# Kernel tuning notes

Hardware: AMD Instinct MI355X
Metric: run time of the kernel (lower is better)

Reference implementation:

```python
import jax, jax.numpy as jnp
import numpy as np

N_NODES = 50000
N_EDGES = 600000
N_FEAT = 128
N_GRAPHS = 256
DIM = 95
N_OUT = 12
N_ITER = 10
BN_EPS = 1e-5


def setup_inputs() -> dict:
    key = jax.random.key(0)
    ks = jax.random.split(key, 16)
    inp = {}
    inp["x"] = jax.random.normal(ks[0], (N_NODES, N_FEAT), dtype=jnp.float32)
    inp["edge_index"] = jax.random.randint(ks[1], (2, N_EDGES), 0, N_NODES, dtype=jnp.int64)
    inp["batch"] = jnp.sort(jax.random.randint(ks[2], (N_NODES,), 0, N_GRAPHS, dtype=jnp.int64))
    def lin(k, fan_in, fan_out):
        bound = 1.0 / np.sqrt(fan_in)
        kw, kb = jax.random.split(k)
        W = jax.random.uniform(kw, (fan_in, fan_out), jnp.float32, -bound, bound)
        b = jax.random.uniform(kb, (fan_out,), jnp.float32, -bound, bound)
        return W, b
    inp["W1a"], inp["b1a"] = lin(ks[3], N_FEAT, N_FEAT)            # nn1 layer 1
    inp["W1b"], inp["b1b"] = lin(ks[4], N_FEAT, N_FEAT)            # nn1 layer 2
    inp["gamma"] = jnp.ones((N_FEAT,), jnp.float32)                 # bn1 weight
    inp["beta"] = jnp.zeros((N_FEAT,), jnp.float32)                 # bn1 bias
    inp["Wl1"], inp["bl1"] = lin(ks[5], 2 * N_FEAT, N_FEAT // 2)   # lin1
    inp["Wl2"], inp["bl2"] = lin(ks[6], 2 * N_FEAT, N_FEAT // 2)   # lin2
    inp["Wm1"], inp["bm1"] = lin(ks[7], N_FEAT, DIM)               # MLP layer 1
    inp["Wm2"], inp["bm2"] = lin(ks[8], DIM, N_OUT)                # MLP layer 2
    return inp


def reference(x, edge_index, batch, W1a, b1a, W1b, b1b, gamma, beta,
              Wl1, bl1, Wl2, bl2, Wm1, bm1, Wm2, bm2):
    src, dst = edge_index[0], edge_index[1]
    # GINConv (eps=0): h_i = nn1(x_i + sum_{j->i} x_j)
    agg = jax.ops.segment_sum(x[src], dst, num_segments=N_NODES)
    h0 = x + agg
    h0 = jax.nn.relu(h0 @ W1a + b1a) @ W1b + b1b
    x1 = jax.nn.relu(h0)
    # BatchNorm1d (training mode: batch statistics, biased variance)
    mean = jnp.mean(x1, axis=0)
    var = jnp.mean(jnp.square(x1 - mean), axis=0)
    x1 = gamma * (x1 - mean) * jax.lax.rsqrt(var + BN_EPS) + beta
    # global_mean_pool over graph ids
    sums = jax.ops.segment_sum(x1, batch, num_segments=N_GRAPHS)
    counts = jax.ops.segment_sum(jnp.ones((N_NODES,), x1.dtype), batch, num_segments=N_GRAPHS)
    xg = sums / jnp.maximum(counts, 1.0)[:, None]
    # recurrent gated loop
    h = xg
    for _ in range(N_ITER):
        cat = jnp.concatenate([xg, h], axis=1)          # [G, 2*F]
        p = cat @ Wl1 + bl1
        q = cat @ Wl2 + bl2
        h = jnp.concatenate([jnp.tanh(q), jax.nn.sigmoid(p)], axis=1)
    # output MLP
    return jax.nn.relu(h @ Wm1 + bm1) @ Wm2 + bm2
```

## Files before the change

kernel.cpp:

```cpp
#include <hip/hip_runtime.h>
#include <cstddef>

#define N_NODES  50000
#define N_EDGES  600000
#define N_FEAT   128
#define N_GRAPHS 256
#define DIMM     95
#define N_OUTD   12
#define N_ITERS  10

#define N_CHUNKS 196

#define WS_BUF   0
#define WS_STATS (N_NODES * N_FEAT)
#define WS_SCALE (WS_STATS + 256)
#define WS_XG    (WS_SCALE + 256)
#define WS_CNT   (WS_XG + N_GRAPHS * N_FEAT)
#define WS_OFF   (WS_CNT + N_NODES)
#define WS_CUR   (WS_OFF + N_NODES + 4)
#define WS_CHS   (WS_CUR + N_NODES)
#define WS_SORT  (WS_CHS + 256)

#define SR 132

__global__ void k_zero(float* __restrict__ ws) {
    int i = blockIdx.x * 256 + threadIdx.x;
    int* cnt = (int*)ws + WS_CNT;
    if (i < N_NODES) cnt[i] = 0;
    if (blockIdx.x == 0) ws[WS_STATS + threadIdx.x] = 0.f;
}

__global__ void k_hist(const int* __restrict__ ei, float* __restrict__ ws) {
    int e = blockIdx.x * 256 + threadIdx.x;
    int* cnt = (int*)ws + WS_CNT;
    if (e < N_EDGES) atomicAdd(&cnt[ei[N_EDGES + e]], 1);
}

__global__ void k_chunk(float* __restrict__ ws) {
    __shared__ int red[4];
    const int tid = threadIdx.x;
    int* cnt = (int*)ws + WS_CNT;
    int i = blockIdx.x * 256 + tid;
    int v = (i < N_NODES) ? cnt[i] : 0;
    #pragma unroll
    for (int d = 32; d; d >>= 1) v += __shfl_down(v, d);
    if ((tid & 63) == 0) red[tid >> 6] = v;
    __syncthreads();
    if (tid == 0) ((int*)ws + WS_CHS)[blockIdx.x] = red[0] + red[1] + red[2] + red[3];
}

__global__ void k_scan0(float* __restrict__ ws) {
    __shared__ int s[256];
    const int tid = threadIdx.x;
    int* chs = (int*)ws + WS_CHS;
    int v = (tid < N_CHUNKS) ? chs[tid] : 0;
    s[tid] = v;
    __syncthreads();
    #pragma unroll
    for (int d = 1; d < 256; d <<= 1) {
        int t = (tid >= d) ? s[tid - d] : 0;
        __syncthreads();
        s[tid] += t;
        __syncthreads();
    }
    if (tid < N_CHUNKS) chs[tid] = s[tid] - v;
    if (tid == 0) ((int*)ws + WS_OFF)[N_NODES] = N_EDGES;
}

__global__ void k_scan1(float* __restrict__ ws) {
    __shared__ int s[256];
    const int tid = threadIdx.x;
    int* cnt = (int*)ws + WS_CNT;
    int* off = (int*)ws + WS_OFF;
    int* cur = (int*)ws + WS_CUR;
    int i = blockIdx.x * 256 + tid;
    int v = (i < N_NODES) ? cnt[i] : 0;
    s[tid] = v;
    __syncthreads();
    #pragma unroll
    for (int d = 1; d < 256; d <<= 1) {
        int t = (tid >= d) ? s[tid - d] : 0;
        __syncthreads();
        s[tid] += t;
        __syncthreads();
    }
    int o = ((int*)ws + WS_CHS)[blockIdx.x] + s[tid] - v;
    if (i < N_NODES) { off[i] = o; cur[i] = o; }
}

__global__ void k_scatter(const int* __restrict__ ei, float* __restrict__ ws) {
    int e = blockIdx.x * 256 + threadIdx.x;
    if (e >= N_EDGES) return;
    int d = ei[N_EDGES + e];
    int s = ei[e];
    int* cur = (int*)ws + WS_CUR;
    int pos = atomicAdd(&cur[d], 1);
    ((int*)ws + WS_SORT)[pos] = s;
}

__global__ __launch_bounds__(256, 4) void k_fused(const float* __restrict__ x,
        float* __restrict__ ws,
        const float* __restrict__ W1a, const float* __restrict__ b1a,
        const float* __restrict__ W1b, const float* __restrict__ b1b) {
    __shared__ float As[64 * SR];
    const int tid  = threadIdx.x;
    const int lane = tid & 63;
    const int wv   = tid >> 6;
    const int fg   = tid & 15;
    const int rg   = tid >> 4;
    const int row0 = blockIdx.x * 64;

    const int* off = (const int*)ws + WS_OFF;
    const int* ss  = (const int*)ws + WS_SORT;

    for (int ii = 0; ii < 16; ++ii) {
        const int i = wv * 16 + ii;
        const int r = row0 + i;
        float a0 = 0.f, a1 = 0.f;
        if (r < N_NODES) {
            a0 = x[(size_t)r * N_FEAT + lane];
            a1 = x[(size_t)r * N_FEAT + 64 + lane];
            const int lo = off[r], hi = off[r + 1];
            int e = lo;
            for (; e + 4 <= hi; e += 4) {
                int s0 = ss[e], s1 = ss[e + 1], s2 = ss[e + 2], s3 = ss[e + 3];
                const float* p0 = x + (size_t)s0 * N_FEAT;
                const float* p1 = x + (size_t)s1 * N_FEAT;
                const float* p2 = x + (size_t)s2 * N_FEAT;
                const float* p3 = x + (size_t)s3 * N_FEAT;
                float u0 = p0[lane], v0 = p0[64 + lane];
                float u1 = p1[lane], v1 = p1[64 + lane];
                float u2 = p2[lane], v2 = p2[64 + lane];
                float u3 = p3[lane], v3 = p3[64 + lane];
                a0 += u0 + u1 + u2 + u3;
                a1 += v0 + v1 + v2 + v3;
            }
            for (; e < hi; ++e) {
                const float* p = x + (size_t)ss[e] * N_FEAT;
                a0 += p[lane];
                a1 += p[64 + lane];
            }
        }
        As[i * SR + lane]      = a0;
        As[i * SR + 64 + lane] = a1;
    }
    __syncthreads();

    float acc[4][8];
    #pragma unroll
    for (int i = 0; i < 4; ++i)
        #pragma unroll
        for (int j = 0; j < 8; ++j) acc[i][j] = 0.f;

    #pragma unroll 2
    for (int k = 0; k < N_FEAT; k += 4) {
        float4 w[8];
        #pragma unroll
        for (int kk = 0; kk < 4; ++kk) {
            w[2 * kk]     = *(const float4*)(W1a + (k + kk) * N_FEAT + fg * 8);
            w[2 * kk + 1] = *(const float4*)(W1a + (k + kk) * N_FEAT + fg * 8 + 4);
        }
        #pragma unroll
        for (int i = 0; i < 4; ++i) {
            const float4 a4 = *(const float4*)(As + (rg * 4 + i) * SR + k);
            const float av[4] = {a4.x, a4.y, a4.z, a4.w};
            #pragma unroll
            for (int kk = 0; kk < 4; ++kk) {
                acc[i][0] += av[kk] * w[2 * kk].x;
                acc[i][1] += av[kk] * w[2 * kk].y;
                acc[i][2] += av[kk] * w[2 * kk].z;
                acc[i][3] += av[kk] * w[2 * kk].w;
                acc[i][4] += av[kk] * w[2 * kk + 1].x;
                acc[i][5] += av[kk] * w[2 * kk + 1].y;
                acc[i][6] += av[kk] * w[2 * kk + 1].z;
                acc[i][7] += av[kk] * w[2 * kk + 1].w;
            }
        }
    }
    __syncthreads();

    {
        const float4 ba0 = *(const float4*)(b1a + fg * 8);
        const float4 ba1 = *(const float4*)(b1a + fg * 8 + 4);
        #pragma unroll
        for (int i = 0; i < 4; ++i) {
            float4 u0, u1;
            u0.x = fmaxf(acc[i][0] + ba0.x, 0.f); u0.y = fmaxf(acc[i][1] + ba0.y, 0.f);
            u0.z = fmaxf(acc[i][2] + ba0.z, 0.f); u0.w = fmaxf(acc[i][3] + ba0.w, 0.f);
            u1.x = fmaxf(acc[i][4] + ba1.x, 0.f); u1.y = fmaxf(acc[i][5] + ba1.y, 0.f);
            u1.z = fmaxf(acc[i][6] + ba1.z, 0.f); u1.w = fmaxf(acc[i][7] + ba1.w, 0.f);
            *(float4*)(As + (rg * 4 + i) * SR + fg * 8)     = u0;
            *(float4*)(As + (rg * 4 + i) * SR + fg * 8 + 4) = u1;
        }
    }
    __syncthreads();

    #pragma unroll
    for (int i = 0; i < 4; ++i)
        #pragma unroll
        for (int j = 0; j < 8; ++j) acc[i][j] = 0.f;

    #pragma unroll 2
    for (int k = 0; k < N_FEAT; k += 4) {
        float4 w[8];
        #pragma unroll
        for (int kk = 0; kk < 4; ++kk) {
            w[2 * kk]     = *(const float4*)(W1b + (k + kk) * N_FEAT + fg * 8);
            w[2 * kk + 1] = *(const float4*)(W1b + (k + kk) * N_FEAT + fg * 8 + 4);
        }
        #pragma unroll
        for (int i = 0; i < 4; ++i) {
            const float4 a4 = *(const float4*)(As + (rg * 4 + i) * SR + k);
            const float av[4] = {a4.x, a4.y, a4.z, a4.w};
            #pragma unroll
            for (int kk = 0; kk < 4; ++kk) {
                acc[i][0] += av[kk] * w[2 * kk].x;
                acc[i][1] += av[kk] * w[2 * kk].y;
                acc[i][2] += av[kk] * w[2 * kk].z;
                acc[i][3] += av[kk] * w[2 * kk].w;
                acc[i][4] += av[kk] * w[2 * kk + 1].x;
                acc[i][5] += av[kk] * w[2 * kk + 1].y;
                acc[i][6] += av[kk] * w[2 * kk + 1].z;
                acc[i][7] += av[kk] * w[2 * kk + 1].w;
            }
        }
    }
    {
        float* __restrict__ buf = ws + WS_BUF;
        const float4 bb0 = *(const float4*)(b1b + fg * 8);
        const float4 bb1 = *(const float4*)(b1b + fg * 8 + 4);
        #pragma unroll
        for (int i = 0; i < 4; ++i) {
            int r = row0 + rg * 4 + i;
            if (r < N_NODES) {
                float4 u0, u1;
                u0.x = fmaxf(acc[i][0] + bb0.x, 0.f); u0.y = fmaxf(acc[i][1] + bb0.y, 0.f);
                u0.z = fmaxf(acc[i][2] + bb0.z, 0.f); u0.w = fmaxf(acc[i][3] + bb0.w, 0.f);
                u1.x = fmaxf(acc[i][4] + bb1.x, 0.f); u1.y = fmaxf(acc[i][5] + bb1.y, 0.f);
                u1.z = fmaxf(acc[i][6] + bb1.z, 0.f); u1.w = fmaxf(acc[i][7] + bb1.w, 0.f);
                *(float4*)(buf + (size_t)r * N_FEAT + fg * 8)     = u0;
                *(float4*)(buf + (size_t)r * N_FEAT + fg * 8 + 4) = u1;
            }
        }
    }
}

__global__ void k_stats(const float* __restrict__ buf, float* __restrict__ stats) {
    __shared__ float S[8][128];
    __shared__ float Q[8][128];
    const int tid = threadIdx.x;
    const int cg = tid & 31;
    const int rg = tid >> 5;
    float4 s = make_float4(0.f, 0.f, 0.f, 0.f);
    float4 q = make_float4(0.f, 0.f, 0.f, 0.f);
    for (int r = blockIdx.x * 8 + rg; r < N_NODES; r += gridDim.x * 8) {
        float4 v = *(const float4*)(buf + (size_t)r * N_FEAT + cg * 4);
        s.x += v.x; s.y += v.y; s.z += v.z; s.w += v.w;
        q.x += v.x * v.x; q.y += v.y * v.y; q.z += v.z * v.z; q.w += v.w * v.w;
    }
    S[rg][cg * 4 + 0] = s.x; S[rg][cg * 4 + 1] = s.y;
    S[rg][cg * 4 + 2] = s.z; S[rg][cg * 4 + 3] = s.w;
    Q[rg][cg * 4 + 0] = q.x; Q[rg][cg * 4 + 1] = q.y;
    Q[rg][cg * 4 + 2] = q.z; Q[rg][cg * 4 + 3] = q.w;
    __syncthreads();
    if (tid < 128) {
        float t = 0.f;
        #pragma unroll
        for (int g = 0; g < 8; ++g) t += S[g][tid];
        unsafeAtomicAdd(stats + tid, t);
    } else {
        int c = tid - 128;
        float t = 0.f;
        #pragma unroll
        for (int g = 0; g < 8; ++g) t += Q[g][c];
        unsafeAtomicAdd(stats + 128 + c, t);
    }
}

__global__ void k_finalize(const float* __restrict__ gamma, const float* __restrict__ beta,
                           float* __restrict__ ws) {
    int c = threadIdx.x;
    float mean = ws[WS_STATS + c] * (1.f / N_NODES);
    float var  = fmaxf(ws[WS_STATS + 128 + c] * (1.f / N_NODES) - mean * mean, 0.f);
    float sc = gamma[c] * rsqrtf(var + 1e-5f);
    ws[WS_SCALE + c] = sc;
    ws[WS_SCALE + 128 + c] = beta[c] - mean * sc;
}

__device__ __forceinline__ int lbound(const int* __restrict__ a, int n, int v) {
    int lo = 0, hi = n;
    while (lo < hi) { int m = (lo + hi) >> 1; if (a[m] < v) lo = m + 1; else hi = m; }
    return lo;
}

__global__ void k_pool(const float* __restrict__ buf, const int* __restrict__ batch,
                       float* __restrict__ ws) {
    __shared__ float S[8][128];
    __shared__ int range[2];
    const int g = blockIdx.x, tid = threadIdx.x;
    if (tid == 0) {
        range[0] = lbound(batch, N_NODES, g);
        range[1] = lbound(batch, N_NODES, g + 1);
    }
    __syncthreads();
    const int lo = range[0], hi = range[1];
    const int cg = tid & 31, rg = tid >> 5;
    float4 s = make_float4(0.f, 0.f, 0.f, 0.f);
    for (int r = lo + rg; r < hi; r += 8) {
        float4 v = *(const float4*)(buf + (size_t)r * N_FEAT + cg * 4);
        s.x += v.x; s.y += v.y; s.z += v.z; s.w += v.w;
    }
    S[rg][cg * 4 + 0] = s.x; S[rg][cg * 4 + 1] = s.y;
    S[rg][cg * 4 + 2] = s.z; S[rg][cg * 4 + 3] = s.w;
    __syncthreads();
    if (tid < 128) {
        float t = 0.f;
        #pragma unroll
        for (int g8 = 0; g8 < 8; ++g8) t += S[g8][tid];
        int cnt = hi - lo;
        float sc = ws[WS_SCALE + tid], sh = ws[WS_SCALE + 128 + tid];
        ws[WS_XG + g * N_FEAT + tid] = (cnt > 0) ? (sc * t / (float)cnt + sh) : 0.f;
    }
}

__global__ __launch_bounds__(256) void k_recur(const float* __restrict__ ws,
        const float* __restrict__ Wl1, const float* __restrict__ bl1,
        const float* __restrict__ Wl2, const float* __restrict__ bl2,
        const float* __restrict__ Wm1, const float* __restrict__ bm1,
        const float* __restrict__ Wm2, const float* __restrict__ bm2,
        float* __restrict__ out) {
    __shared__ float W1h[128 * 64];
    __shared__ float W2h[128 * 64];
    __shared__ float xg_s[128];
    __shared__ float h_s[128];
    __shared__ float px[2][64];
    __shared__ float pq[2][2][64];
    __shared__ float m_s[DIMM];
    const int g = blockIdx.x, tid = threadIdx.x;

    for (int i = tid; i < 128 * 64; i += 256) {
        W1h[i] = Wl1[128 * 64 + i];
        W2h[i] = Wl2[128 * 64 + i];
    }
    if (tid < 128) {
        float v = ws[WS_XG + g * N_FEAT + tid];
        xg_s[tid] = v;
        h_s[tid] = v;
    }
    __syncthreads();

    const int sel  = tid >> 7;
    const int part = (tid >> 6) & 1;
    const int j    = tid & 63;

    {
        const float* Wg = sel ? Wl2 : Wl1;
        float a = 0.f;
        const int k0 = part * 64;
        #pragma unroll 4
        for (int k = 0; k < 64; ++k) a += xg_s[k0 + k] * Wg[(k0 + k) * 64 + j];
        pq[sel][part][j] = a;
    }
    __syncthreads();
    if (part == 0) {
        const float* bias = sel ? bl2 : bl1;
        px[sel][j] = pq[sel][0][j] + pq[sel][1][j] + bias[j];
    }
    __syncthreads();

    const float* Wh = sel ? W2h : W1h;
    for (int it = 0; it < N_ITERS; ++it) {
        float a = 0.f;
        const int k0 = part * 64;
        #pragma unroll
        for (int k = 0; k < 64; k += 4) {
            const float4 h4 = *(const float4*)(h_s + k0 + k);
            a += h4.x * Wh[(k0 + k + 0) * 64 + j];
            a += h4.y * Wh[(k0 + k + 1) * 64 + j];
            a += h4.z * Wh[(k0 + k + 2) * 64 + j];
            a += h4.w * Wh[(k0 + k + 3) * 64 + j];
        }
        pq[sel][part][j] = a;
        __syncthreads();
        if (part == 0) {
            float tot = pq[sel][0][j] + pq[sel][1][j] + px[sel][j];
            if (sel == 0) h_s[64 + j] = 1.f / (1.f + expf(-tot));
            else          h_s[j] = tanhf(tot);
        }
        __syncthreads();
    }

    if (tid < DIMM) {
        float a = bm1[tid];
        #pragma unroll 4
        for (int k = 0; k < 128; ++k) a += h_s[k] * Wm1[k * DIMM + tid];
        m_s[tid] = fmaxf(a, 0.f);
    }
    __syncthreads();
    if (tid < N_OUTD) {
        float a = bm2[tid];
        for (int k = 0; k < DIMM; ++k) a += m_s[k] * Wm2[k * N_OUTD + tid];
        out[g * N_OUTD + tid] = a;
    }
}

extern "C" void kernel_launch(void* const* d_in, const int* in_sizes, int n_in,
                              void* d_out, int out_size, void* d_ws, size_t ws_size,
                              hipStream_t stream) {
    const float* x     = (const float*)d_in[0];
    const int*   ei    = (const int*)d_in[1];
    const int*   batch = (const int*)d_in[2];
    const float* W1a = (const float*)d_in[3];
    const float* b1a = (const float*)d_in[4];
    const float* W1b = (const float*)d_in[5];
    const float* b1b = (const float*)d_in[6];
    const float* gamma = (const float*)d_in[7];
    const float* beta  = (const float*)d_in[8];
    const float* Wl1 = (const float*)d_in[9];
    const float* bl1 = (const float*)d_in[10];
    const float* Wl2 = (const float*)d_in[11];
    const float* bl2 = (const float*)d_in[12];
    const float* Wm1 = (const float*)d_in[13];
    const float* bm1 = (const float*)d_in[14];
    const float* Wm2 = (const float*)d_in[15];
    const float* bm2 = (const float*)d_in[16];
    float* out = (float*)d_out;
    float* ws  = (float*)d_ws;

    k_zero   <<<(N_NODES + 255) / 256, 256, 0, stream>>>(ws);
    k_hist   <<<(N_EDGES + 255) / 256, 256, 0, stream>>>(ei, ws);
    k_chunk  <<<N_CHUNKS, 256, 0, stream>>>(ws);
    k_scan0  <<<1, 256, 0, stream>>>(ws);
    k_scan1  <<<N_CHUNKS, 256, 0, stream>>>(ws);
    k_scatter<<<(N_EDGES + 255) / 256, 256, 0, stream>>>(ei, ws);
    k_fused  <<<(N_NODES + 63) / 64, 256, 0, stream>>>(x, ws, W1a, b1a, W1b, b1b);
    k_stats  <<<512, 256, 0, stream>>>(ws + WS_BUF, ws + WS_STATS);
    k_finalize<<<1, 128, 0, stream>>>(gamma, beta, ws);
    k_pool   <<<N_GRAPHS, 256, 0, stream>>>(ws + WS_BUF, batch, ws);
    k_recur  <<<N_GRAPHS, 256, 0, stream>>>(ws, Wl1, bl1, Wl2, bl2, Wm1, bm1, Wm2, bm2, out);
}
```

Baseline: 342.2 us.

## Fuse BN statistics and mean pooling into GIN MLP kernel epilogue

The fused gather+MLP kernel no longer writes the 50000x128 activation buffer. Its epilogue stages the tile in shared memory, accumulates per-feature sum and sum-of-squares, and pools per-graph sums with atomics. BN scale/shift is then applied to the pooled sums in a small kernel, which replaces the separate stats, finalize and pool passes. The gather loop also loads neighbor indices cooperatively per wave with shuffles and float2 loads. This adds atomics and an extra sync, and applying BN after pooling relies on its linearity.

```diff
diff --git a/kernel.cpp b/kernel.cpp
--- a/kernel.cpp
+++ b/kernel.cpp
@@ -11,10 +11,8 @@
 
 #define N_CHUNKS 196
 
-#define WS_BUF   0
-#define WS_STATS (N_NODES * N_FEAT)
-#define WS_SCALE (WS_STATS + 256)
-#define WS_XG    (WS_SCALE + 256)
+#define WS_STATS 0
+#define WS_XG    (WS_STATS + 256)
 #define WS_CNT   (WS_XG + N_GRAPHS * N_FEAT)
 #define WS_OFF   (WS_CNT + N_NODES)
 #define WS_CUR   (WS_OFF + N_NODES + 4)
@@ -27,7 +25,8 @@
     int i = blockIdx.x * 256 + threadIdx.x;
     int* cnt = (int*)ws + WS_CNT;
     if (i < N_NODES) cnt[i] = 0;
-    if (blockIdx.x == 0) ws[WS_STATS + threadIdx.x] = 0.f;
+    if (i < 256) ws[WS_STATS + i] = 0.f;
+    if (i < N_GRAPHS * N_FEAT) ws[WS_XG + i] = 0.f;
 }
 
 __global__ void k_hist(const int* __restrict__ ei, float* __restrict__ ws) {
@@ -99,10 +98,12 @@
 }
 
 __global__ __launch_bounds__(256, 4) void k_fused(const float* __restrict__ x,
-        float* __restrict__ ws,
+        const int* __restrict__ batch, float* __restrict__ ws,
         const float* __restrict__ W1a, const float* __restrict__ b1a,
         const float* __restrict__ W1b, const float* __restrict__ b1b) {
     __shared__ float As[64 * SR];
+    __shared__ float red[256];
+    __shared__ int batch_l[64];
     const int tid  = threadIdx.x;
     const int lane = tid & 63;
     const int wv   = tid >> 6;
@@ -113,36 +114,42 @@
     const int* off = (const int*)ws + WS_OFF;
     const int* ss  = (const int*)ws + WS_SORT;
 
+    if (tid < 64) {
+        int r = row0 + tid;
+        batch_l[tid] = (r < N_NODES) ? batch[r] : (N_GRAPHS - 1);
+    }
+
     for (int ii = 0; ii < 16; ++ii) {
         const int i = wv * 16 + ii;
         const int r = row0 + i;
-        float a0 = 0.f, a1 = 0.f;
+        float2 acc = make_float2(0.f, 0.f);
         if (r < N_NODES) {
-            a0 = x[(size_t)r * N_FEAT + lane];
-            a1 = x[(size_t)r * N_FEAT + 64 + lane];
+            acc = *(const float2*)(x + (size_t)r * N_FEAT + 2 * lane);
             const int lo = off[r], hi = off[r + 1];
-            int e = lo;
-            for (; e + 4 <= hi; e += 4) {
-                int s0 = ss[e], s1 = ss[e + 1], s2 = ss[e + 2], s3 = ss[e + 3];
-                const float* p0 = x + (size_t)s0 * N_FEAT;
-                const float* p1 = x + (size_t)s1 * N_FEAT;
-                const float* p2 = x + (size_t)s2 * N_FEAT;
-                const float* p3 = x + (size_t)s3 * N_FEAT;
-                float u0 = p0[lane], v0 = p0[64 + lane];
-                float u1 = p1[lane], v1 = p1[64 + lane];
-                float u2 = p2[lane], v2 = p2[64 + lane];
-                float u3 = p3[lane], v3 = p3[64 + lane];
-                a0 += u0 + u1 + u2 + u3;
-                a1 += v0 + v1 + v2 + v3;
+            for (int c0 = lo; c0 < hi; c0 += 64) {
+                const int cdeg = min(64, hi - c0);
+                int myidx = (lane < cdeg) ? ss[c0 + lane] : 0;
+                int j = 0;
+                for (; j + 4 <= cdeg; j += 4) {
+                    int s0 = __shfl(myidx, j);
+                    int s1 = __shfl(myidx, j + 1);
+                    int s2 = __shfl(myidx, j + 2);
+                    int s3 = __shfl(myidx, j + 3);
+                    float2 v0 = *(const float2*)(x + (size_t)s0 * N_FEAT + 2 * lane);
+                    float2 v1 = *(const float2*)(x + (size_t)s1 * N_FEAT + 2 * lane);
+                    float2 v2 = *(const float2*)(x + (size_t)s2 * N_FEAT + 2 * lane);
+                    float2 v3 = *(const float2*)(x + (size_t)s3 * N_FEAT + 2 * lane);
+                    acc.x += v0.x + v1.x + v2.x + v3.x;
+                    acc.y += v0.y + v1.y + v2.y + v3.y;
+                }
+                for (; j < cdeg; ++j) {
+                    int s = __shfl(myidx, j);
+                    float2 v = *(const float2*)(x + (size_t)s * N_FEAT + 2 * lane);
+                    acc.x += v.x; acc.y += v.y;
+                }
             }
-            for (; e < hi; ++e) {
-                const float* p = x + (size_t)ss[e] * N_FEAT;
-                a0 += p[lane];
-                a1 += p[64 + lane];
-            }
-        }
-        As[i * SR + lane]      = a0;
-        As[i * SR + 64 + lane] = a1;
+        }
+        *(float2*)(As + i * SR + 2 * lane) = acc;
     }
     __syncthreads();
 
@@ -225,66 +232,50 @@
             }
         }
     }
+    __syncthreads();
+
     {
-        float* __restrict__ buf = ws + WS_BUF;
         const float4 bb0 = *(const float4*)(b1b + fg * 8);
         const float4 bb1 = *(const float4*)(b1b + fg * 8 + 4);
         #pragma unroll
         for (int i = 0; i < 4; ++i) {
-            int r = row0 + rg * 4 + i;
-            if (r < N_NODES) {
-                float4 u0, u1;
-                u0.x = fmaxf(acc[i][0] + bb0.x, 0.f); u0.y = fmaxf(acc[i][1] + bb0.y, 0.f);
-                u0.z = fmaxf(acc[i][2] + bb0.z, 0.f); u0.w = fmaxf(acc[i][3] + bb0.w, 0.f);
-                u1.x = fmaxf(acc[i][4] + bb1.x, 0.f); u1.y = fmaxf(acc[i][5] + bb1.y, 0.f);
-                u1.z = fmaxf(acc[i][6] + bb1.z, 0.f); u1.w = fmaxf(acc[i][7] + bb1.w, 0.f);
-                *(float4*)(buf + (size_t)r * N_FEAT + fg * 8)     = u0;
-                *(float4*)(buf + (size_t)r * N_FEAT + fg * 8 + 4) = u1;
+            float4 u0, u1;
+            u0.x = fmaxf(acc[i][0] + bb0.x, 0.f); u0.y = fmaxf(acc[i][1] + bb0.y, 0.f);
+            u0.z = fmaxf(acc[i][2] + bb0.z, 0.f); u0.w = fmaxf(acc[i][3] + bb0.w, 0.f);
+            u1.x = fmaxf(acc[i][4] + bb1.x, 0.f); u1.y = fmaxf(acc[i][5] + bb1.y, 0.f);
+            u1.z = fmaxf(acc[i][6] + bb1.z, 0.f); u1.w = fmaxf(acc[i][7] + bb1.w, 0.f);
+            *(float4*)(As + (rg * 4 + i) * SR + fg * 8)     = u0;
+            *(float4*)(As + (rg * 4 + i) * SR + fg * 8 + 4) = u1;
+        }
+    }
+    __syncthreads();
+
+    {
+        const int c = tid & 127;
+        const int h = tid >> 7;
+        float sum = 0.f, sq = 0.f, pool = 0.f;
+        int curg = batch_l[h * 32];
+        bool any = (row0 + h * 32) < N_NODES;
+        #pragma unroll 4
+        for (int rr = 0; rr < 32; ++rr) {
+            int rl = h * 32 + rr;
+            if (row0 + rl >= N_NODES) break;
+            float v = As[rl * SR + c];
+            int g = batch_l[rl];
+            if (g != curg) {
+                unsafeAtomicAdd(ws + WS_XG + (size_t)curg * N_FEAT + c, pool);
+                pool = 0.f; curg = g;
             }
-        }
-    }
-}
-
-__global__ void k_stats(const float* __restrict__ buf, float* __restrict__ stats) {
-    __shared__ float S[8][128];
-    __shared__ float Q[8][128];
-    const int tid = threadIdx.x;
-    const int cg = tid & 31;
-    const int rg = tid >> 5;
-    float4 s = make_float4(0.f, 0.f, 0.f, 0.f);
-    float4 q = make_float4(0.f, 0.f, 0.f, 0.f);
-    for (int r = blockIdx.x * 8 + rg; r < N_NODES; r += gridDim.x * 8) {
-        float4 v = *(const float4*)(buf + (size_t)r * N_FEAT + cg * 4);
-        s.x += v.x; s.y += v.y; s.z += v.z; s.w += v.w;
-        q.x += v.x * v.x; q.y += v.y * v.y; q.z += v.z * v.z; q.w += v.w * v.w;
-    }
-    S[rg][cg * 4 + 0] = s.x; S[rg][cg * 4 + 1] = s.y;
-    S[rg][cg * 4 + 2] = s.z; S[rg][cg * 4 + 3] = s.w;
-    Q[rg][cg * 4 + 0] = q.x; Q[rg][cg * 4 + 1] = q.y;
-    Q[rg][cg * 4 + 2] = q.z; Q[rg][cg * 4 + 3] = q.w;
-    __syncthreads();
-    if (tid < 128) {
-        float t = 0.f;
-        #pragma unroll
-        for (int g = 0; g < 8; ++g) t += S[g][tid];
-        unsafeAtomicAdd(stats + tid, t);
-    } else {
-        int c = tid - 128;
-        float t = 0.f;
-        #pragma unroll
-        for (int g = 0; g < 8; ++g) t += Q[g][c];
-        unsafeAtomicAdd(stats + 128 + c, t);
-    }
-}
-
-__global__ void k_finalize(const float* __restrict__ gamma, const float* __restrict__ beta,
-                           float* __restrict__ ws) {
-    int c = threadIdx.x;
-    float mean = ws[WS_STATS + c] * (1.f / N_NODES);
-    float var  = fmaxf(ws[WS_STATS + 128 + c] * (1.f / N_NODES) - mean * mean, 0.f);
-    float sc = gamma[c] * rsqrtf(var + 1e-5f);
-    ws[WS_SCALE + c] = sc;
-    ws[WS_SCALE + 128 + c] = beta[c] - mean * sc;
+            sum += v; sq += v * v; pool += v;
+        }
+        if (any) unsafeAtomicAdd(ws + WS_XG + (size_t)curg * N_FEAT + c, pool);
+        if (h == 1) { red[c] = sum; red[128 + c] = sq; }
+        __syncthreads();
+        if (h == 0) {
+            unsafeAtomicAdd(ws + WS_STATS + c, sum + red[c]);
+            unsafeAtomicAdd(ws + WS_STATS + 128 + c, sq + red[128 + c]);
+        }
+    }
 }
 
 __device__ __forceinline__ int lbound(const int* __restrict__ a, int n, int v) {
@@ -293,34 +284,20 @@
     return lo;
 }
 
-__global__ void k_pool(const float* __restrict__ buf, const int* __restrict__ batch,
-                       float* __restrict__ ws) {
-    __shared__ float S[8][128];
+__global__ void k_apply(const int* __restrict__ batch,
+                        const float* __restrict__ gamma, const float* __restrict__ beta,
+                        float* __restrict__ ws) {
+    const int g = blockIdx.x, c = threadIdx.x;
     __shared__ int range[2];
-    const int g = blockIdx.x, tid = threadIdx.x;
-    if (tid == 0) {
-        range[0] = lbound(batch, N_NODES, g);
-        range[1] = lbound(batch, N_NODES, g + 1);
-    }
-    __syncthreads();
-    const int lo = range[0], hi = range[1];
-    const int cg = tid & 31, rg = tid >> 5;
-    float4 s = make_float4(0.f, 0.f, 0.f, 0.f);
-    for (int r = lo + rg; r < hi; r += 8) {
-        float4 v = *(const float4*)(buf + (size_t)r * N_FEAT + cg * 4);
-        s.x += v.x; s.y += v.y; s.z += v.z; s.w += v.w;
-    }
-    S[rg][cg * 4 + 0] = s.x; S[rg][cg * 4 + 1] = s.y;
-    S[rg][cg * 4 + 2] = s.z; S[rg][cg * 4 + 3] = s.w;
-    __syncthreads();
-    if (tid < 128) {
-        float t = 0.f;
-        #pragma unroll
-        for (int g8 = 0; g8 < 8; ++g8) t += S[g8][tid];
-        int cnt = hi - lo;
-        float sc = ws[WS_SCALE + tid], sh = ws[WS_SCALE + 128 + tid];
-        ws[WS_XG + g * N_FEAT + tid] = (cnt > 0) ? (sc * t / (float)cnt + sh) : 0.f;
-    }
+    if (c < 2) range[c] = lbound(batch, N_NODES, g + c);
+    __syncthreads();
+    const int cnt = range[1] - range[0];
+    float mean = ws[WS_STATS + c] * (1.f / N_NODES);
+    float var  = fmaxf(ws[WS_STATS + 128 + c] * (1.f / N_NODES) - mean * mean, 0.f);
+    float sc = gamma[c] * rsqrtf(var + 1e-5f);
+    float sh = beta[c] - mean * sc;
+    float pool = ws[WS_XG + (size_t)g * N_FEAT + c];
+    ws[WS_XG + (size_t)g * N_FEAT + c] = (cnt > 0) ? (sc * pool / (float)cnt + sh) : 0.f;
 }
 
 __global__ __launch_bounds__(256) void k_recur(const float* __restrict__ ws,
@@ -433,9 +410,7 @@
     k_scan0  <<<1, 256, 0, stream>>>(ws);
     k_scan1  <<<N_CHUNKS, 256, 0, stream>>>(ws);
     k_scatter<<<(N_EDGES + 255) / 256, 256, 0, stream>>>(ei, ws);
-    k_fused  <<<(N_NODES + 63) / 64, 256, 0, stream>>>(x, ws, W1a, b1a, W1b, b1b);
-    k_stats  <<<512, 256, 0, stream>>>(ws + WS_BUF, ws + WS_STATS);
-    k_finalize<<<1, 128, 0, stream>>>(gamma, beta, ws);
-    k_pool   <<<N_GRAPHS, 256, 0, stream>>>(ws + WS_BUF, batch, ws);
+    k_fused  <<<(N_NODES + 63) / 64, 256, 0, stream>>>(x, batch, ws, W1a, b1a, W1b, b1b);
+    k_apply  <<<N_GRAPHS, 128, 0, stream>>>(batch, gamma, beta, ws);
     k_recur  <<<N_GRAPHS, 256, 0, stream>>>(ws, Wl1, bl1, Wl2, bl2, Wm1, bm1, Wm2, bm2, out);
 }
```

Result: faster. 311.9 us (-8.9%).
